# Performance work log

Measured on AMD Instinct MI355X. Metric: run time of the kernel, lower is better.

Reference implementation:

```python
import jax, jax.numpy as jnp
import numpy as np

B, D, H = 262144, 250, 100  # batch, input_length, hidden_length


def setup_inputs() -> dict:
    key = jax.random.key(0)
    ks = jax.random.split(key, 20)
    s_in = 1.0 / np.sqrt(D)
    s_h = 1.0 / np.sqrt(H)
    inp = {
        "x": jax.random.normal(ks[0], (B, D), jnp.float32),
        "h_prev": jax.random.normal(ks[1], (B, H), jnp.float32),
        "h_shared_prev": jax.random.normal(ks[2], (B, H), jnp.float32),
        # shared nn.GRUCell(D, H) params (torch layout: weight_ih [3H, D], weight_hh [3H, H])
        "Wi": jax.random.uniform(ks[3], (3 * H, D), jnp.float32, -s_in, s_in),
        "Wh": jax.random.uniform(ks[4], (3 * H, H), jnp.float32, -s_h, s_h),
        "bi": jax.random.uniform(ks[5], (3 * H,), jnp.float32, -s_h, s_h),
        "bh": jax.random.uniform(ks[6], (3 * H,), jnp.float32, -s_h, s_h),
        # task-specific bias-free linears, torch nn.Linear layout [out, in]
        "W_z": jax.random.uniform(ks[7], (H, D), jnp.float32, -s_in, s_in),
        "U_z": jax.random.uniform(ks[8], (H, H), jnp.float32, -s_h, s_h),
        "Us_z": jax.random.uniform(ks[9], (H, H), jnp.float32, -s_h, s_h),
        "W_r": jax.random.uniform(ks[10], (H, D), jnp.float32, -s_in, s_in),
        "U_r": jax.random.uniform(ks[11], (H, H), jnp.float32, -s_h, s_h),
        "Us_r": jax.random.uniform(ks[12], (H, H), jnp.float32, -s_h, s_h),
        "W_hn": jax.random.uniform(ks[13], (H, D), jnp.float32, -s_in, s_in),
        "U_hn": jax.random.uniform(ks[14], (H, H), jnp.float32, -s_h, s_h),
        "Us_hn": jax.random.uniform(ks[15], (H, H), jnp.float32, -s_h, s_h),
    }
    return inp


def _shared_gru_cell(x, h, Wi, Wh, bi, bh):
    # standard torch nn.GRUCell math
    gi = x @ Wi.T + bi          # [B, 3H]
    gh = h @ Wh.T + bh          # [B, 3H]
    i_r, i_z, i_n = jnp.split(gi, 3, axis=-1)
    h_r, h_z, h_n = jnp.split(gh, 3, axis=-1)
    r = jax.nn.sigmoid(i_r + h_r)
    z = jax.nn.sigmoid(i_z + h_z)
    n = jnp.tanh(i_n + r * h_n)
    return (1.0 - z) * n + z * h


def reference(x, h_prev, h_shared_prev, Wi, Wh, bi, bh,
              W_z, U_z, Us_z, W_r, U_r, Us_r, W_hn, U_hn, Us_hn):
    h_shared_new = _shared_gru_cell(x, h_shared_prev, Wi, Wh, bi, bh)
    z = jax.nn.sigmoid(x @ W_z.T + h_prev @ U_z.T + h_shared_new @ Us_z.T)
    r = jax.nn.sigmoid(x @ W_r.T + h_prev @ U_r.T + h_shared_new @ Us_r.T)
    nm = jnp.tanh(x @ W_hn.T + r * (h_prev @ U_hn.T) + h_shared_new @ Us_hn.T)
    h_new = (1.0 - z) * nm + z * h_prev
    return h_new
```

## Files before the change

kernel.cpp:

```cpp
#include <hip/hip_runtime.h>
#include <stdint.h>

#define D_IN 250
#define H_DIM 100
#define RPW 32
#define NTHREADS 256
#define BM (4*RPW)

#define P2_FRAG 252
#define TOTAL_E ((252 + 336) * 512)

typedef __bf16 bf16x8 __attribute__((ext_vector_type(8)));
typedef float f32x4 __attribute__((ext_vector_type(4)));

static __device__ __forceinline__ uint16_t f2bf(float f) {
  uint32_t u = __builtin_bit_cast(uint32_t, f);
  u = (u + 0x7FFFu + ((u >> 16) & 1u)) >> 16;
  return (uint16_t)u;
}
static __device__ __forceinline__ float bf2f(uint16_t h) {
  uint32_t u = ((uint32_t)h) << 16;
  return __builtin_bit_cast(float, u);
}
static __device__ __forceinline__ float sigmoidf_(float x) {
  return 1.0f / (1.0f + __expf(-x));
}
static __device__ __forceinline__ float tanhf_(float x) {
  return 2.0f / (1.0f + __expf(-2.0f * x)) - 1.0f;
}

__global__ void prepack_kernel(const float* __restrict__ Wi, const float* __restrict__ Wh,
                               const float* __restrict__ W_z, const float* __restrict__ U_z,
                               const float* __restrict__ Us_z, const float* __restrict__ W_r,
                               const float* __restrict__ U_r, const float* __restrict__ Us_r,
                               const float* __restrict__ W_hn, const float* __restrict__ U_hn,
                               const float* __restrict__ Us_hn, const float* __restrict__ bi,
                               const float* __restrict__ bh, uint16_t* __restrict__ ws) {
  int idx = blockIdx.x * blockDim.x + threadIdx.x;
  if (idx >= TOTAL_E) return;
  int f = idx >> 9;
  int a = idx & 511;
  int lane = a >> 3, j = a & 7;
  int kloc = ((lane >> 4) << 3) + j;
  int cl = lane & 15;
  float val = 0.f;
  if (f < P2_FRAG) {
    int g = f % 3, ks = (f / 3) % 12, t = f / 36;
    int c = t * 16 + cl;
    if (c < H_DIM) {
      if (ks < 8) {
        int k = ks * 32 + kloc;
        if (k < D_IN)       val = Wi[(size_t)(g * H_DIM + c) * D_IN + k];
        else if (k == D_IN) val = bi[g * H_DIM + c];
      } else {
        int k = (ks - 8) * 32 + kloc;
        if (k < H_DIM)       val = Wh[(size_t)(g * H_DIM + c) * H_DIM + k];
        else if (k == H_DIM) val = bh[g * H_DIM + c];
      }
    }
  } else {
    int f2 = f - P2_FRAG;
    int g = f2 % 3, ks = (f2 / 3) % 16, t = f2 / 48;
    int c = t * 16 + cl;
    if (c < H_DIM) {
      if (ks < 8) {
        int k = ks * 32 + kloc;
        const float* W = g == 0 ? W_z : g == 1 ? W_r : W_hn;
        if (k < D_IN) val = W[(size_t)c * D_IN + k];
      } else if (ks < 12) {
        int k = (ks - 8) * 32 + kloc;
        const float* W = g == 0 ? U_z : g == 1 ? U_r : U_hn;
        if (k < H_DIM) val = W[(size_t)c * H_DIM + k];
      } else {
        int k = (ks - 12) * 32 + kloc;
        const float* W = g == 0 ? Us_z : g == 1 ? Us_r : Us_hn;
        if (k < H_DIM) val = W[(size_t)c * H_DIM + k];
      }
    }
  }
  ws[idx] = f2bf(val);
}

static __device__ __forceinline__ bf16x8 xfrag(const float* __restrict__ xr, int ks, int q) {
  int c0 = ks * 32 + q * 8;
  bf16x8 a;
  if (c0 < 248) {
    #pragma unroll
    for (int i = 0; i < 4; ++i) {
      float2 f = *(const float2*)(xr + c0 + 2 * i);
      a[2 * i] = (__bf16)f.x; a[2 * i + 1] = (__bf16)f.y;
    }
  } else {
    float2 f = *(const float2*)(xr + 248);
    a[0] = (__bf16)f.x; a[1] = (__bf16)f.y; a[2] = (__bf16)1.0f;
    a[3] = (__bf16)0.0f; a[4] = (__bf16)0.0f; a[5] = (__bf16)0.0f;
    a[6] = (__bf16)0.0f; a[7] = (__bf16)0.0f;
  }
  return a;
}
static __device__ __forceinline__ bf16x8 hfrag(const float* __restrict__ hr, int ks, int q, float bias) {
  int c0 = ks * 32 + q * 8;
  bf16x8 a;
  #pragma unroll
  for (int i = 0; i < 8; ++i) a[i] = (__bf16)0.0f;
  if (c0 <= 88) {
    #pragma unroll
    for (int i = 0; i < 4; ++i) {
      float2 f = *(const float2*)(hr + c0 + 2 * i);
      a[2 * i] = (__bf16)f.x; a[2 * i + 1] = (__bf16)f.y;
    }
  } else if (c0 == 96) {
    float2 f0 = *(const float2*)(hr + 96);
    float2 f1 = *(const float2*)(hr + 98);
    a[0] = (__bf16)f0.x; a[1] = (__bf16)f0.y; a[2] = (__bf16)f1.x; a[3] = (__bf16)f1.y;
    a[4] = (__bf16)bias;
  }
  return a;
}

#define MFMA(A, B, C) __builtin_amdgcn_mfma_f32_16x16x32_bf16((A), (B), (C), 0, 0, 0)

typedef const __attribute__((address_space(1))) unsigned int* gp1_t;
typedef __attribute__((address_space(3))) unsigned int* lp3_t;

static __device__ __forceinline__ void gload(const uint16_t* gsrc, uint16_t* ldst) {
  __builtin_amdgcn_global_load_lds((gp1_t)gsrc, (lp3_t)ldst, 16, 0, 0);
}
#define WAIT_VM5   asm volatile("s_waitcnt vmcnt(5)" ::: "memory")
#define WAIT_LGKM0 asm volatile("s_waitcnt lgkmcnt(0)" ::: "memory")
#define BAR        do { __builtin_amdgcn_s_barrier(); __builtin_amdgcn_sched_barrier(0); } while (0)

__global__ __launch_bounds__(NTHREADS, 2) void gru_fused(
    const float* __restrict__ x, const float* __restrict__ hp_g,
    const float* __restrict__ hs_g, const uint16_t* __restrict__ ws,
    float* __restrict__ out) {
  __shared__ __align__(16) uint16_t ldsT[4 * RPW * 128];
  __shared__ __align__(16) uint16_t ring[8 * 1536];

  const int tid = threadIdx.x;
  const int lane = tid & 63, wid = tid >> 6;
  const int q = lane >> 4, cl = lane & 15;
  const int rowbase = blockIdx.x * BM + wid * RPW;
  uint16_t* lT = ldsT + wid * (RPW * 128);
  const uint16_t* wsl = ws + lane * 8;

  bf16x8 xa[2][8], ha[2][4], pa[2][4];
  #pragma unroll
  for (int h = 0; h < 2; ++h) {
    const float* xr = x + (size_t)(rowbase + h * 16 + cl) * D_IN;
    #pragma unroll
    for (int ks = 0; ks < 8; ++ks) xa[h][ks] = xfrag(xr, ks, q);
    const float* hr = hs_g + (size_t)(rowbase + h * 16 + cl) * H_DIM;
    #pragma unroll
    for (int ks = 0; ks < 4; ++ks) ha[h][ks] = hfrag(hr, ks, q, 1.0f);
    const float* pr = hp_g + (size_t)(rowbase + h * 16 + cl) * H_DIM;
    #pragma unroll
    for (int ks = 0; ks < 4; ++ks) pa[h][ks] = hfrag(pr, ks, q, 0.0f);
  }

  #pragma unroll
  for (int h = 0; h < 2; ++h) {
    int row = h * 16 + cl;
    #pragma unroll
    for (int ks = 0; ks < 4; ++ks) {
      int bo = row * 256 + (((ks * 64) + q * 16) ^ ((row & 7) << 4));
      *(bf16x8*)((char*)lT + bo) = ha[h][ks];
    }
  }

  if (wid < 3) {
    #pragma unroll
    for (int s = 0; s < 6; ++s)
      gload(wsl + (size_t)(s * 3 + wid) * 512, ring + s * 1536 + wid * 512);
    WAIT_VM5;
  }
  BAR;

  #pragma unroll 1
  for (int t = 0; t < 7; ++t) {
    f32x4 aR[2], aZ[2], aNi[2], aNh[2];
    #pragma unroll
    for (int h = 0; h < 2; ++h) { aR[h] = (f32x4)(0.f); aZ[h] = (f32x4)(0.f); aNi[h] = (f32x4)(0.f); aNh[h] = (f32x4)(0.f); }
    #pragma unroll
    for (int ks = 0; ks < 12; ++ks) {
      const uint16_t* sp = ring + ((t * 12 + ks) & 7) * 1536 + lane * 8;
      bf16x8 b0 = *(const bf16x8*)(sp);
      bf16x8 b1 = *(const bf16x8*)(sp + 512);
      bf16x8 b2 = *(const bf16x8*)(sp + 1024);
      if (wid < 3) {
        int fid = (ks < 6) ? (t * 36 + (ks + 6) * 3)
                : (t < 6 ? ((t + 1) * 36 + (ks - 6) * 3) : (P2_FRAG + (ks - 6) * 3));
        gload(wsl + (size_t)(fid + wid) * 512,
              ring + ((t * 12 + ks + 6) & 7) * 1536 + wid * 512);
      }
      #pragma unroll
      for (int h = 0; h < 2; ++h) {
        bf16x8 av = (ks < 8) ? xa[h][ks] : ha[h][ks - 8];
        aR[h] = MFMA(av, b0, aR[h]);
        aZ[h] = MFMA(av, b1, aZ[h]);
        if (ks < 8) aNi[h] = MFMA(av, b2, aNi[h]);
        else        aNh[h] = MFMA(av, b2, aNh[h]);
      }
      if (wid < 3) WAIT_VM5;
      BAR;
    }
    int c = t * 16 + cl;
    #pragma unroll
    for (int h = 0; h < 2; ++h) {
      #pragma unroll
      for (int r = 0; r < 4; ++r) {
        int row = h * 16 + q * 4 + r;
        int bo = row * 256 + ((c * 2) ^ ((row & 7) << 4));
        float hsp = bf2f(*(const uint16_t*)((const char*)lT + bo));
        float rr = sigmoidf_(aR[h][r]);
        float zz = sigmoidf_(aZ[h][r]);
        float nn = tanhf_(aNi[h][r] + rr * aNh[h][r]);
        float hsn = (1.f - zz) * nn + zz * hsp;
        *(uint16_t*)((char*)lT + bo) = f2bf(hsn);
      }
    }
  }

  bf16x8 na[2][4];
  #pragma unroll
  for (int h = 0; h < 2; ++h) {
    int row = h * 16 + cl;
    #pragma unroll
    for (int ks = 0; ks < 4; ++ks) {
      int bo = row * 256 + (((ks * 64) + q * 16) ^ ((row & 7) << 4));
      na[h][ks] = *(const bf16x8*)((const char*)lT + bo);
    }
  }
  WAIT_LGKM0;
  #pragma unroll
  for (int h = 0; h < 2; ++h) {
    int row = h * 16 + cl;
    #pragma unroll
    for (int ks = 0; ks < 4; ++ks) {
      int bo = row * 256 + (((ks * 64) + q * 16) ^ ((row & 7) << 4));
      *(bf16x8*)((char*)lT + bo) = pa[h][ks];
    }
  }

  #pragma unroll 1
  for (int t = 0; t < 7; ++t) {
    f32x4 aZ[2], aR[2], aNa[2], aNb[2];
    #pragma unroll
    for (int h = 0; h < 2; ++h) { aZ[h] = (f32x4)(0.f); aR[h] = (f32x4)(0.f); aNa[h] = (f32x4)(0.f); aNb[h] = (f32x4)(0.f); }
    #pragma unroll
    for (int ks = 0; ks < 16; ++ks) {
      const uint16_t* sp = ring + ((84 + t * 16 + ks) & 7) * 1536 + lane * 8;
      bf16x8 b0 = *(const bf16x8*)(sp);
      bf16x8 b1 = *(const bf16x8*)(sp + 512);
      bf16x8 b2 = *(const bf16x8*)(sp + 1024);
      if (wid < 3) {
        int fid = (ks < 10) ? (P2_FRAG + t * 48 + (ks + 6) * 3)
                : (t < 6 ? (P2_FRAG + (t + 1) * 48 + (ks - 10) * 3)
                         : (P2_FRAG + 6 * 48 + 15 * 3));
        gload(wsl + (size_t)(fid + wid) * 512,
              ring + ((84 + t * 16 + ks + 6) & 7) * 1536 + wid * 512);
      }
      #pragma unroll
      for (int h = 0; h < 2; ++h) {
        bf16x8 av = (ks < 8) ? xa[h][ks] : (ks < 12) ? pa[h][ks - 8] : na[h][ks - 12];
        aZ[h] = MFMA(av, b0, aZ[h]);
        aR[h] = MFMA(av, b1, aR[h]);
        if (ks < 8)       aNa[h] = MFMA(av, b2, aNa[h]);
        else if (ks < 12) aNb[h] = MFMA(av, b2, aNb[h]);
        else              aNa[h] = MFMA(av, b2, aNa[h]);
      }
      if (wid < 3) WAIT_VM5;
      BAR;
    }
    int c = t * 16 + cl;
    bool valid = c < H_DIM;
    #pragma unroll
    for (int h = 0; h < 2; ++h) {
      #pragma unroll
      for (int r = 0; r < 4; ++r) {
        int row = h * 16 + q * 4 + r;
        int bo = row * 256 + ((c * 2) ^ ((row & 7) << 4));
        float hpv = bf2f(*(const uint16_t*)((const char*)lT + bo));
        float z2 = sigmoidf_(aZ[h][r]);
        float r2 = sigmoidf_(aR[h][r]);
        float nm = tanhf_(aNa[h][r] + r2 * aNb[h][r]);
        float hnew = (1.f - z2) * nm + z2 * hpv;
        if (valid) out[(size_t)(rowbase + row) * H_DIM + c] = hnew;
      }
    }
  }
}

extern "C" void kernel_launch(void* const* d_in, const int* in_sizes, int n_in,
                              void* d_out, int out_size, void* d_ws, size_t ws_size,
                              hipStream_t stream) {
  const float* x    = (const float*)d_in[0];
  const float* h_p  = (const float*)d_in[1];
  const float* h_s  = (const float*)d_in[2];
  const float* Wi   = (const float*)d_in[3];
  const float* Wh   = (const float*)d_in[4];
  const float* bi   = (const float*)d_in[5];
  const float* bh   = (const float*)d_in[6];
  const float* W_z  = (const float*)d_in[7];
  const float* U_z  = (const float*)d_in[8];
  const float* Us_z = (const float*)d_in[9];
  const float* W_r  = (const float*)d_in[10];
  const float* U_r  = (const float*)d_in[11];
  const float* Us_r = (const float*)d_in[12];
  const float* W_hn = (const float*)d_in[13];
  const float* U_hn = (const float*)d_in[14];
  const float* Us_hn= (const float*)d_in[15];
  uint16_t* ws = (uint16_t*)d_ws;
  float* out = (float*)d_out;

  int rows = in_sizes[0] / D_IN;
  prepack_kernel<<<(TOTAL_E + 255) / 256, 256, 0, stream>>>(
      Wi, Wh, W_z, U_z, Us_z, W_r, U_r, Us_r, W_hn, U_hn, Us_hn, bi, bh, ws);
  gru_fused<<<rows / BM, NTHREADS, 0, stream>>>(x, h_p, h_s, ws, out);
}
```

Baseline: 272.0 us.

## Shrink weight ring to six slots, pair k-steps per barrier, raise occupancy

```diff
diff --git a/kernel.cpp b/kernel.cpp
--- a/kernel.cpp
+++ b/kernel.cpp
@@ -9,6 +9,8 @@
 
 #define P2_FRAG 252
 #define TOTAL_E ((252 + 336) * 512)
+
+#define NSLOT 6
 
 typedef __bf16 bf16x8 __attribute__((ext_vector_type(8)));
 typedef float f32x4 __attribute__((ext_vector_type(4)));
@@ -126,16 +128,21 @@
 static __device__ __forceinline__ void gload(const uint16_t* gsrc, uint16_t* ldst) {
   __builtin_amdgcn_global_load_lds((gp1_t)gsrc, (lp3_t)ldst, 16, 0, 0);
 }
-#define WAIT_VM5   asm volatile("s_waitcnt vmcnt(5)" ::: "memory")
+#define WAIT_VM2   asm volatile("s_waitcnt vmcnt(2)" ::: "memory")
 #define WAIT_LGKM0 asm volatile("s_waitcnt lgkmcnt(0)" ::: "memory")
 #define BAR        do { __builtin_amdgcn_s_barrier(); __builtin_amdgcn_sched_barrier(0); } while (0)
 
-__global__ __launch_bounds__(NTHREADS, 2) void gru_fused(
+static __device__ __forceinline__ int adv(int s, int n) {
+  s += n;
+  return s >= NSLOT ? s - NSLOT : s;
+}
+
+__global__ __launch_bounds__(NTHREADS, 3) void gru_fused(
     const float* __restrict__ x, const float* __restrict__ hp_g,
     const float* __restrict__ hs_g, const uint16_t* __restrict__ ws,
     float* __restrict__ out) {
   __shared__ __align__(16) uint16_t ldsT[4 * RPW * 128];
-  __shared__ __align__(16) uint16_t ring[8 * 1536];
+  __shared__ __align__(16) uint16_t ring[NSLOT * 1536];
 
   const int tid = threadIdx.x;
   const int lane = tid & 63, wid = tid >> 6;
@@ -170,11 +177,13 @@
 
   if (wid < 3) {
     #pragma unroll
-    for (int s = 0; s < 6; ++s)
+    for (int s = 0; s < 4; ++s)
       gload(wsl + (size_t)(s * 3 + wid) * 512, ring + s * 1536 + wid * 512);
-    WAIT_VM5;
+    WAIT_VM2;
   }
   BAR;
+
+  int cslot = 0, islot = 4;
 
   #pragma unroll 1
   for (int t = 0; t < 7; ++t) {
@@ -182,26 +191,48 @@
     #pragma unroll
     for (int h = 0; h < 2; ++h) { aR[h] = (f32x4)(0.f); aZ[h] = (f32x4)(0.f); aNi[h] = (f32x4)(0.f); aNh[h] = (f32x4)(0.f); }
     #pragma unroll
-    for (int ks = 0; ks < 12; ++ks) {
-      const uint16_t* sp = ring + ((t * 12 + ks) & 7) * 1536 + lane * 8;
-      bf16x8 b0 = *(const bf16x8*)(sp);
-      bf16x8 b1 = *(const bf16x8*)(sp + 512);
-      bf16x8 b2 = *(const bf16x8*)(sp + 1024);
+    for (int ks = 0; ks < 12; ks += 2) {
+      int c0s = cslot, c1s = adv(cslot, 1);
+      const uint16_t* spa = ring + c0s * 1536 + lane * 8;
+      bf16x8 a0 = *(const bf16x8*)(spa);
+      bf16x8 a1 = *(const bf16x8*)(spa + 512);
+      bf16x8 a2 = *(const bf16x8*)(spa + 1024);
       if (wid < 3) {
-        int fid = (ks < 6) ? (t * 36 + (ks + 6) * 3)
-                : (t < 6 ? ((t + 1) * 36 + (ks - 6) * 3) : (P2_FRAG + (ks - 6) * 3));
-        gload(wsl + (size_t)(fid + wid) * 512,
-              ring + ((t * 12 + ks + 6) & 7) * 1536 + wid * 512);
-      }
+        int f1 = (ks + 4 < 12) ? (t * 36 + (ks + 4) * 3)
+               : (t < 6 ? ((t + 1) * 36 + (ks - 8) * 3) : (P2_FRAG + (ks - 8) * 3));
+        gload(wsl + (size_t)(f1 + wid) * 512, ring + islot * 1536 + wid * 512);
+      }
+      __builtin_amdgcn_s_setprio(1);
       #pragma unroll
       for (int h = 0; h < 2; ++h) {
         bf16x8 av = (ks < 8) ? xa[h][ks] : ha[h][ks - 8];
+        aR[h] = MFMA(av, a0, aR[h]);
+        aZ[h] = MFMA(av, a1, aZ[h]);
+        if (ks < 8) aNi[h] = MFMA(av, a2, aNi[h]);
+        else        aNh[h] = MFMA(av, a2, aNh[h]);
+      }
+      __builtin_amdgcn_s_setprio(0);
+      const uint16_t* spb = ring + c1s * 1536 + lane * 8;
+      bf16x8 b0 = *(const bf16x8*)(spb);
+      bf16x8 b1 = *(const bf16x8*)(spb + 512);
+      bf16x8 b2 = *(const bf16x8*)(spb + 1024);
+      if (wid < 3) {
+        int f2_ = (ks + 5 < 12) ? (t * 36 + (ks + 5) * 3)
+                : (t < 6 ? ((t + 1) * 36 + (ks - 7) * 3) : (P2_FRAG + (ks - 7) * 3));
+        gload(wsl + (size_t)(f2_ + wid) * 512, ring + adv(islot, 1) * 1536 + wid * 512);
+      }
+      __builtin_amdgcn_s_setprio(1);
+      #pragma unroll
+      for (int h = 0; h < 2; ++h) {
+        bf16x8 av = (ks + 1 < 8) ? xa[h][ks + 1] : ha[h][ks + 1 - 8];
         aR[h] = MFMA(av, b0, aR[h]);
         aZ[h] = MFMA(av, b1, aZ[h]);
-        if (ks < 8) aNi[h] = MFMA(av, b2, aNi[h]);
-        else        aNh[h] = MFMA(av, b2, aNh[h]);
-      }
-      if (wid < 3) WAIT_VM5;
+        if (ks + 1 < 8) aNi[h] = MFMA(av, b2, aNi[h]);
+        else            aNh[h] = MFMA(av, b2, aNh[h]);
+      }
+      __builtin_amdgcn_s_setprio(0);
+      cslot = adv(cslot, 2); islot = adv(islot, 2);
+      if (wid < 3) WAIT_VM2;
       BAR;
     }
     int c = t * 16 + cl;
@@ -248,28 +279,50 @@
     #pragma unroll
     for (int h = 0; h < 2; ++h) { aZ[h] = (f32x4)(0.f); aR[h] = (f32x4)(0.f); aNa[h] = (f32x4)(0.f); aNb[h] = (f32x4)(0.f); }
     #pragma unroll
-    for (int ks = 0; ks < 16; ++ks) {
-      const uint16_t* sp = ring + ((84 + t * 16 + ks) & 7) * 1536 + lane * 8;
-      bf16x8 b0 = *(const bf16x8*)(sp);
-      bf16x8 b1 = *(const bf16x8*)(sp + 512);
-      bf16x8 b2 = *(const bf16x8*)(sp + 1024);
+    for (int ks = 0; ks < 16; ks += 2) {
+      int c0s = cslot, c1s = adv(cslot, 1);
+      const uint16_t* spa = ring + c0s * 1536 + lane * 8;
+      bf16x8 a0 = *(const bf16x8*)(spa);
+      bf16x8 a1 = *(const bf16x8*)(spa + 512);
+      bf16x8 a2 = *(const bf16x8*)(spa + 1024);
       if (wid < 3) {
-        int fid = (ks < 10) ? (P2_FRAG + t * 48 + (ks + 6) * 3)
-                : (t < 6 ? (P2_FRAG + (t + 1) * 48 + (ks - 10) * 3)
-                         : (P2_FRAG + 6 * 48 + 15 * 3));
-        gload(wsl + (size_t)(fid + wid) * 512,
-              ring + ((84 + t * 16 + ks + 6) & 7) * 1536 + wid * 512);
-      }
+        int f1 = (ks + 4 < 16) ? (P2_FRAG + t * 48 + (ks + 4) * 3)
+               : (t < 6 ? (P2_FRAG + (t + 1) * 48 + (ks - 12) * 3) : (P2_FRAG + 6 * 48 + 45));
+        gload(wsl + (size_t)(f1 + wid) * 512, ring + islot * 1536 + wid * 512);
+      }
+      __builtin_amdgcn_s_setprio(1);
       #pragma unroll
       for (int h = 0; h < 2; ++h) {
         bf16x8 av = (ks < 8) ? xa[h][ks] : (ks < 12) ? pa[h][ks - 8] : na[h][ks - 12];
+        aZ[h] = MFMA(av, a0, aZ[h]);
+        aR[h] = MFMA(av, a1, aR[h]);
+        if (ks < 8)       aNa[h] = MFMA(av, a2, aNa[h]);
+        else if (ks < 12) aNb[h] = MFMA(av, a2, aNb[h]);
+        else              aNa[h] = MFMA(av, a2, aNa[h]);
+      }
+      __builtin_amdgcn_s_setprio(0);
+      const uint16_t* spb = ring + c1s * 1536 + lane * 8;
+      bf16x8 b0 = *(const bf16x8*)(spb);
+      bf16x8 b1 = *(const bf16x8*)(spb + 512);
+      bf16x8 b2 = *(const bf16x8*)(spb + 1024);
+      if (wid < 3) {
+        int f2_ = (ks + 5 < 16) ? (P2_FRAG + t * 48 + (ks + 5) * 3)
+                : (t < 6 ? (P2_FRAG + (t + 1) * 48 + (ks - 11) * 3) : (P2_FRAG + 6 * 48 + 45));
+        gload(wsl + (size_t)(f2_ + wid) * 512, ring + adv(islot, 1) * 1536 + wid * 512);
+      }
+      __builtin_amdgcn_s_setprio(1);
+      #pragma unroll
+      for (int h = 0; h < 2; ++h) {
+        bf16x8 av = (ks + 1 < 8) ? xa[h][ks + 1] : (ks + 1 < 12) ? pa[h][ks + 1 - 8] : na[h][ks + 1 - 12];
         aZ[h] = MFMA(av, b0, aZ[h]);
         aR[h] = MFMA(av, b1, aR[h]);
-        if (ks < 8)       aNa[h] = MFMA(av, b2, aNa[h]);
-        else if (ks < 12) aNb[h] = MFMA(av, b2, aNb[h]);
-        else              aNa[h] = MFMA(av, b2, aNa[h]);
-      }
-      if (wid < 3) WAIT_VM5;
+        if (ks + 1 < 8)       aNa[h] = MFMA(av, b2, aNa[h]);
+        else if (ks + 1 < 12) aNb[h] = MFMA(av, b2, aNb[h]);
+        else                  aNa[h] = MFMA(av, b2, aNa[h]);
+      }
+      __builtin_amdgcn_s_setprio(0);
+      cslot = adv(cslot, 2); islot = adv(islot, 2);
+      if (wid < 3) WAIT_VM2;
       BAR;
     }
     int c = t * 16 + cl;
```

New measurement: 497.5 us. 82.9% more time.

## Restructure weight ring to 12 slots with grouped 4-step stages and fewer barriers

Applied to the files above, without the earlier changes.

```diff
diff --git a/kernel.cpp b/kernel.cpp
--- a/kernel.cpp
+++ b/kernel.cpp
@@ -9,6 +9,8 @@
 
 #define P2_FRAG 252
 #define TOTAL_E ((252 + 336) * 512)
+
+#define NSLOT 12
 
 typedef __bf16 bf16x8 __attribute__((ext_vector_type(8)));
 typedef float f32x4 __attribute__((ext_vector_type(4)));
@@ -126,7 +128,7 @@
 static __device__ __forceinline__ void gload(const uint16_t* gsrc, uint16_t* ldst) {
   __builtin_amdgcn_global_load_lds((gp1_t)gsrc, (lp3_t)ldst, 16, 0, 0);
 }
-#define WAIT_VM5   asm volatile("s_waitcnt vmcnt(5)" ::: "memory")
+#define WAIT_VM3   asm volatile("s_waitcnt vmcnt(3)" ::: "memory")
 #define WAIT_LGKM0 asm volatile("s_waitcnt lgkmcnt(0)" ::: "memory")
 #define BAR        do { __builtin_amdgcn_s_barrier(); __builtin_amdgcn_sched_barrier(0); } while (0)
 
@@ -135,7 +137,7 @@
     const float* __restrict__ hs_g, const uint16_t* __restrict__ ws,
     float* __restrict__ out) {
   __shared__ __align__(16) uint16_t ldsT[4 * RPW * 128];
-  __shared__ __align__(16) uint16_t ring[8 * 1536];
+  __shared__ __align__(16) uint16_t ring[NSLOT * 1536];
 
   const int tid = threadIdx.x;
   const int lane = tid & 63, wid = tid >> 6;
@@ -168,11 +170,16 @@
     }
   }
 
-  if (wid < 3) {
-    #pragma unroll
-    for (int s = 0; s < 6; ++s)
-      gload(wsl + (size_t)(s * 3 + wid) * 512, ring + s * 1536 + wid * 512);
-    WAIT_VM5;
+  {
+    int f0 = wid * 3;
+    #pragma unroll
+    for (int gg = 0; gg < 3; ++gg)
+      gload(wsl + (size_t)(f0 + gg) * 512, ring + wid * 1536 + gg * 512);
+    int f1 = (4 + wid) * 3;
+    #pragma unroll
+    for (int gg = 0; gg < 3; ++gg)
+      gload(wsl + (size_t)(f1 + gg) * 512, ring + (4 + wid) * 1536 + gg * 512);
+    WAIT_VM3;
   }
   BAR;
 
@@ -182,26 +189,34 @@
     #pragma unroll
     for (int h = 0; h < 2; ++h) { aR[h] = (f32x4)(0.f); aZ[h] = (f32x4)(0.f); aNi[h] = (f32x4)(0.f); aNh[h] = (f32x4)(0.f); }
     #pragma unroll
-    for (int ks = 0; ks < 12; ++ks) {
-      const uint16_t* sp = ring + ((t * 12 + ks) & 7) * 1536 + lane * 8;
-      bf16x8 b0 = *(const bf16x8*)(sp);
-      bf16x8 b1 = *(const bf16x8*)(sp + 512);
-      bf16x8 b2 = *(const bf16x8*)(sp + 1024);
-      if (wid < 3) {
-        int fid = (ks < 6) ? (t * 36 + (ks + 6) * 3)
-                : (t < 6 ? ((t + 1) * 36 + (ks - 6) * 3) : (P2_FRAG + (ks - 6) * 3));
-        gload(wsl + (size_t)(fid + wid) * 512,
-              ring + ((t * 12 + ks + 6) & 7) * 1536 + wid * 512);
-      }
-      #pragma unroll
-      for (int h = 0; h < 2; ++h) {
-        bf16x8 av = (ks < 8) ? xa[h][ks] : ha[h][ks - 8];
-        aR[h] = MFMA(av, b0, aR[h]);
-        aZ[h] = MFMA(av, b1, aZ[h]);
-        if (ks < 8) aNi[h] = MFMA(av, b2, aNi[h]);
-        else        aNh[h] = MFMA(av, b2, aNh[h]);
-      }
-      if (wid < 3) WAIT_VM5;
+    for (int g = 0; g < 3; ++g) {
+      int islot = (g == 0) ? (8 + wid) : (g == 1) ? wid : (4 + wid);
+      int fid;
+      if (g == 0)      fid = t * 36 + (8 + wid) * 3;
+      else if (g == 1) fid = (t < 6) ? ((t + 1) * 36 + wid * 3) : (P2_FRAG + wid * 3);
+      else             fid = (t < 6) ? ((t + 1) * 36 + (4 + wid) * 3) : (P2_FRAG + (4 + wid) * 3);
+      #pragma unroll
+      for (int gg = 0; gg < 3; ++gg)
+        gload(wsl + (size_t)(fid + gg) * 512, ring + islot * 1536 + gg * 512);
+      #pragma unroll
+      for (int so = 0; so < 4; ++so) {
+        const int ks = 4 * g + so;
+        const uint16_t* sp = ring + ks * 1536 + lane * 8;
+        bf16x8 b0 = *(const bf16x8*)(sp);
+        bf16x8 b1 = *(const bf16x8*)(sp + 512);
+        bf16x8 b2 = *(const bf16x8*)(sp + 1024);
+        __builtin_amdgcn_s_setprio(1);
+        #pragma unroll
+        for (int h = 0; h < 2; ++h) {
+          bf16x8 av = (ks < 8) ? xa[h][ks] : ha[h][ks - 8];
+          aR[h] = MFMA(av, b0, aR[h]);
+          aZ[h] = MFMA(av, b1, aZ[h]);
+          if (ks < 8) aNi[h] = MFMA(av, b2, aNi[h]);
+          else        aNh[h] = MFMA(av, b2, aNh[h]);
+        }
+        __builtin_amdgcn_s_setprio(0);
+      }
+      WAIT_VM3;
       BAR;
     }
     int c = t * 16 + cl;
@@ -242,34 +257,49 @@
     }
   }
 
+  int sb = 0;
   #pragma unroll 1
   for (int t = 0; t < 7; ++t) {
     f32x4 aZ[2], aR[2], aNa[2], aNb[2];
     #pragma unroll
     for (int h = 0; h < 2; ++h) { aZ[h] = (f32x4)(0.f); aR[h] = (f32x4)(0.f); aNa[h] = (f32x4)(0.f); aNb[h] = (f32x4)(0.f); }
     #pragma unroll
-    for (int ks = 0; ks < 16; ++ks) {
-      const uint16_t* sp = ring + ((84 + t * 16 + ks) & 7) * 1536 + lane * 8;
-      bf16x8 b0 = *(const bf16x8*)(sp);
-      bf16x8 b1 = *(const bf16x8*)(sp + 512);
-      bf16x8 b2 = *(const bf16x8*)(sp + 1024);
-      if (wid < 3) {
-        int fid = (ks < 10) ? (P2_FRAG + t * 48 + (ks + 6) * 3)
-                : (t < 6 ? (P2_FRAG + (t + 1) * 48 + (ks - 10) * 3)
-                         : (P2_FRAG + 6 * 48 + 15 * 3));
-        gload(wsl + (size_t)(fid + wid) * 512,
-              ring + ((84 + t * 16 + ks + 6) & 7) * 1536 + wid * 512);
-      }
-      #pragma unroll
-      for (int h = 0; h < 2; ++h) {
-        bf16x8 av = (ks < 8) ? xa[h][ks] : (ks < 12) ? pa[h][ks - 8] : na[h][ks - 12];
-        aZ[h] = MFMA(av, b0, aZ[h]);
-        aR[h] = MFMA(av, b1, aR[h]);
-        if (ks < 8)       aNa[h] = MFMA(av, b2, aNa[h]);
-        else if (ks < 12) aNb[h] = MFMA(av, b2, aNb[h]);
-        else              aNa[h] = MFMA(av, b2, aNa[h]);
-      }
-      if (wid < 3) WAIT_VM5;
+    for (int g = 0; g < 4; ++g) {
+      int fid;
+      if (g == 0)      fid = P2_FRAG + t * 48 + (8 + wid) * 3;
+      else if (g == 1) fid = P2_FRAG + t * 48 + (12 + wid) * 3;
+      else if (g == 2) fid = (t < 6) ? (P2_FRAG + (t + 1) * 48 + wid * 3) : P2_FRAG;
+      else             fid = (t < 6) ? (P2_FRAG + (t + 1) * 48 + (4 + wid) * 3) : P2_FRAG;
+      int islot = sb + 4 * g + 8 + wid;
+      if (islot >= NSLOT) islot -= NSLOT;
+      if (islot >= NSLOT) islot -= NSLOT;
+      #pragma unroll
+      for (int gg = 0; gg < 3; ++gg)
+        gload(wsl + (size_t)(fid + gg) * 512, ring + islot * 1536 + gg * 512);
+      int cb = sb + 4 * g;
+      if (cb >= NSLOT) cb -= NSLOT;
+      #pragma unroll
+      for (int so = 0; so < 4; ++so) {
+        const int ks = 4 * g + so;
+        int sl = cb + so;
+        if (sl >= NSLOT) sl -= NSLOT;
+        const uint16_t* sp = ring + sl * 1536 + lane * 8;
+        bf16x8 b0 = *(const bf16x8*)(sp);
+        bf16x8 b1 = *(const bf16x8*)(sp + 512);
+        bf16x8 b2 = *(const bf16x8*)(sp + 1024);
+        __builtin_amdgcn_s_setprio(1);
+        #pragma unroll
+        for (int h = 0; h < 2; ++h) {
+          bf16x8 av = (ks < 8) ? xa[h][ks] : (ks < 12) ? pa[h][ks - 8] : na[h][ks - 12];
+          aZ[h] = MFMA(av, b0, aZ[h]);
+          aR[h] = MFMA(av, b1, aR[h]);
+          if (ks < 8)       aNa[h] = MFMA(av, b2, aNa[h]);
+          else if (ks < 12) aNb[h] = MFMA(av, b2, aNb[h]);
+          else              aNa[h] = MFMA(av, b2, aNa[h]);
+        }
+        __builtin_amdgcn_s_setprio(0);
+      }
+      WAIT_VM3;
       BAR;
     }
     int c = t * 16 + cl;
@@ -288,6 +318,8 @@
         if (valid) out[(size_t)(rowbase + row) * H_DIM + c] = hnew;
       }
     }
+    sb += 4;
+    if (sb >= NSLOT) sb -= NSLOT;
   }
 }
 
```

After: 306.1 us. 1.13x slower.

## Double-buffer weight fragments in registers and halve barriers per K-step

Applied to the files above, without the earlier changes.

```diff
diff --git a/kernel.cpp b/kernel.cpp
--- a/kernel.cpp
+++ b/kernel.cpp
@@ -9,6 +9,8 @@
 
 #define P2_FRAG 252
 #define TOTAL_E ((252 + 336) * 512)
+
+#define NSLOT 8
 
 typedef __bf16 bf16x8 __attribute__((ext_vector_type(8)));
 typedef float f32x4 __attribute__((ext_vector_type(4)));
@@ -126,7 +128,8 @@
 static __device__ __forceinline__ void gload(const uint16_t* gsrc, uint16_t* ldst) {
   __builtin_amdgcn_global_load_lds((gp1_t)gsrc, (lp3_t)ldst, 16, 0, 0);
 }
-#define WAIT_VM5   asm volatile("s_waitcnt vmcnt(5)" ::: "memory")
+#define WAIT_VM2   asm volatile("s_waitcnt vmcnt(2)" ::: "memory")
+#define WAIT_VM0   asm volatile("s_waitcnt vmcnt(0)" ::: "memory")
 #define WAIT_LGKM0 asm volatile("s_waitcnt lgkmcnt(0)" ::: "memory")
 #define BAR        do { __builtin_amdgcn_s_barrier(); __builtin_amdgcn_sched_barrier(0); } while (0)
 
@@ -135,7 +138,7 @@
     const float* __restrict__ hs_g, const uint16_t* __restrict__ ws,
     float* __restrict__ out) {
   __shared__ __align__(16) uint16_t ldsT[4 * RPW * 128];
-  __shared__ __align__(16) uint16_t ring[8 * 1536];
+  __shared__ __align__(16) uint16_t ring[NSLOT * 1536];
 
   const int tid = threadIdx.x;
   const int lane = tid & 63, wid = tid >> 6;
@@ -172,36 +175,57 @@
     #pragma unroll
     for (int s = 0; s < 6; ++s)
       gload(wsl + (size_t)(s * 3 + wid) * 512, ring + s * 1536 + wid * 512);
-    WAIT_VM5;
+    WAIT_VM2;
   }
   BAR;
+
+  bf16x8 c00, c01, c02, c10, c11, c12;
+  {
+    const uint16_t* sp0 = ring + 0 * 1536 + lane * 8;
+    const uint16_t* sp1 = ring + 1 * 1536 + lane * 8;
+    c00 = *(const bf16x8*)(sp0); c01 = *(const bf16x8*)(sp0 + 512); c02 = *(const bf16x8*)(sp0 + 1024);
+    c10 = *(const bf16x8*)(sp1); c11 = *(const bf16x8*)(sp1 + 512); c12 = *(const bf16x8*)(sp1 + 1024);
+  }
 
   #pragma unroll 1
   for (int t = 0; t < 7; ++t) {
+    const int tb = (t & 1) << 2;
     f32x4 aR[2], aZ[2], aNi[2], aNh[2];
     #pragma unroll
     for (int h = 0; h < 2; ++h) { aR[h] = (f32x4)(0.f); aZ[h] = (f32x4)(0.f); aNi[h] = (f32x4)(0.f); aNh[h] = (f32x4)(0.f); }
     #pragma unroll
-    for (int ks = 0; ks < 12; ++ks) {
-      const uint16_t* sp = ring + ((t * 12 + ks) & 7) * 1536 + lane * 8;
-      bf16x8 b0 = *(const bf16x8*)(sp);
-      bf16x8 b1 = *(const bf16x8*)(sp + 512);
-      bf16x8 b2 = *(const bf16x8*)(sp + 1024);
+    for (int ks = 0; ks < 12; ks += 2) {
       if (wid < 3) {
-        int fid = (ks < 6) ? (t * 36 + (ks + 6) * 3)
-                : (t < 6 ? ((t + 1) * 36 + (ks - 6) * 3) : (P2_FRAG + (ks - 6) * 3));
-        gload(wsl + (size_t)(fid + wid) * 512,
-              ring + ((t * 12 + ks + 6) & 7) * 1536 + wid * 512);
-      }
+        const int k6 = ks + 6, k7 = ks + 7;
+        int f6 = (k6 < 12) ? (t * 36 + k6 * 3)
+               : (t < 6 ? ((t + 1) * 36 + (k6 - 12) * 3) : (P2_FRAG + (k6 - 12) * 3));
+        int f7 = (k7 < 12) ? (t * 36 + k7 * 3)
+               : (t < 6 ? ((t + 1) * 36 + (k7 - 12) * 3) : (P2_FRAG + (k7 - 12) * 3));
+        gload(wsl + (size_t)(f6 + wid) * 512, ring + ((tb + ks + 6) & 7) * 1536 + wid * 512);
+        gload(wsl + (size_t)(f7 + wid) * 512, ring + ((tb + ks + 7) & 7) * 1536 + wid * 512);
+      }
+      __builtin_amdgcn_s_setprio(1);
       #pragma unroll
       for (int h = 0; h < 2; ++h) {
-        bf16x8 av = (ks < 8) ? xa[h][ks] : ha[h][ks - 8];
-        aR[h] = MFMA(av, b0, aR[h]);
-        aZ[h] = MFMA(av, b1, aZ[h]);
-        if (ks < 8) aNi[h] = MFMA(av, b2, aNi[h]);
-        else        aNh[h] = MFMA(av, b2, aNh[h]);
-      }
-      if (wid < 3) WAIT_VM5;
+        bf16x8 av0 = (ks < 8) ? xa[h][ks] : ha[h][ks - 8];
+        aR[h] = MFMA(av0, c00, aR[h]);
+        aZ[h] = MFMA(av0, c01, aZ[h]);
+        if (ks < 8) aNi[h] = MFMA(av0, c02, aNi[h]);
+        else        aNh[h] = MFMA(av0, c02, aNh[h]);
+        bf16x8 av1 = (ks + 1 < 8) ? xa[h][ks + 1] : ha[h][ks + 1 - 8];
+        aR[h] = MFMA(av1, c10, aR[h]);
+        aZ[h] = MFMA(av1, c11, aZ[h]);
+        if (ks + 1 < 8) aNi[h] = MFMA(av1, c12, aNi[h]);
+        else            aNh[h] = MFMA(av1, c12, aNh[h]);
+      }
+      __builtin_amdgcn_s_setprio(0);
+      {
+        const uint16_t* sp0 = ring + ((tb + ks + 2) & 7) * 1536 + lane * 8;
+        const uint16_t* sp1 = ring + ((tb + ks + 3) & 7) * 1536 + lane * 8;
+        c00 = *(const bf16x8*)(sp0); c01 = *(const bf16x8*)(sp0 + 512); c02 = *(const bf16x8*)(sp0 + 1024);
+        c10 = *(const bf16x8*)(sp1); c11 = *(const bf16x8*)(sp1 + 512); c12 = *(const bf16x8*)(sp1 + 1024);
+      }
+      if (wid < 3) WAIT_VM2;
       BAR;
     }
     int c = t * 16 + cl;
@@ -248,28 +272,40 @@
     #pragma unroll
     for (int h = 0; h < 2; ++h) { aZ[h] = (f32x4)(0.f); aR[h] = (f32x4)(0.f); aNa[h] = (f32x4)(0.f); aNb[h] = (f32x4)(0.f); }
     #pragma unroll
-    for (int ks = 0; ks < 16; ++ks) {
-      const uint16_t* sp = ring + ((84 + t * 16 + ks) & 7) * 1536 + lane * 8;
-      bf16x8 b0 = *(const bf16x8*)(sp);
-      bf16x8 b1 = *(const bf16x8*)(sp + 512);
-      bf16x8 b2 = *(const bf16x8*)(sp + 1024);
+    for (int ks = 0; ks < 16; ks += 2) {
       if (wid < 3) {
-        int fid = (ks < 10) ? (P2_FRAG + t * 48 + (ks + 6) * 3)
-                : (t < 6 ? (P2_FRAG + (t + 1) * 48 + (ks - 10) * 3)
-                         : (P2_FRAG + 6 * 48 + 15 * 3));
-        gload(wsl + (size_t)(fid + wid) * 512,
-              ring + ((84 + t * 16 + ks + 6) & 7) * 1536 + wid * 512);
-      }
+        const int k6 = ks + 6, k7 = ks + 7;
+        int f6 = (k6 < 16) ? (P2_FRAG + t * 48 + k6 * 3)
+               : (t < 6 ? (P2_FRAG + (t + 1) * 48 + (k6 - 16) * 3) : P2_FRAG);
+        int f7 = (k7 < 16) ? (P2_FRAG + t * 48 + k7 * 3)
+               : (t < 6 ? (P2_FRAG + (t + 1) * 48 + (k7 - 16) * 3) : P2_FRAG);
+        gload(wsl + (size_t)(f6 + wid) * 512, ring + ((4 + ks + 6) & 7) * 1536 + wid * 512);
+        gload(wsl + (size_t)(f7 + wid) * 512, ring + ((4 + ks + 7) & 7) * 1536 + wid * 512);
+      }
+      __builtin_amdgcn_s_setprio(1);
       #pragma unroll
       for (int h = 0; h < 2; ++h) {
-        bf16x8 av = (ks < 8) ? xa[h][ks] : (ks < 12) ? pa[h][ks - 8] : na[h][ks - 12];
-        aZ[h] = MFMA(av, b0, aZ[h]);
-        aR[h] = MFMA(av, b1, aR[h]);
-        if (ks < 8)       aNa[h] = MFMA(av, b2, aNa[h]);
-        else if (ks < 12) aNb[h] = MFMA(av, b2, aNb[h]);
-        else              aNa[h] = MFMA(av, b2, aNa[h]);
-      }
-      if (wid < 3) WAIT_VM5;
+        bf16x8 av0 = (ks < 8) ? xa[h][ks] : (ks < 12) ? pa[h][ks - 8] : na[h][ks - 12];
+        aZ[h] = MFMA(av0, c00, aZ[h]);
+        aR[h] = MFMA(av0, c01, aR[h]);
+        if (ks < 8)       aNa[h] = MFMA(av0, c02, aNa[h]);
+        else if (ks < 12) aNb[h] = MFMA(av0, c02, aNb[h]);
+        else              aNa[h] = MFMA(av0, c02, aNa[h]);
+        bf16x8 av1 = (ks + 1 < 8) ? xa[h][ks + 1] : (ks + 1 < 12) ? pa[h][ks + 1 - 8] : na[h][ks + 1 - 12];
+        aZ[h] = MFMA(av1, c10, aZ[h]);
+        aR[h] = MFMA(av1, c11, aR[h]);
+        if (ks + 1 < 8)       aNa[h] = MFMA(av1, c12, aNa[h]);
+        else if (ks + 1 < 12) aNb[h] = MFMA(av1, c12, aNb[h]);
+        else                  aNa[h] = MFMA(av1, c12, aNa[h]);
+      }
+      __builtin_amdgcn_s_setprio(0);
+      {
+        const uint16_t* sp0 = ring + ((4 + ks + 2) & 7) * 1536 + lane * 8;
+        const uint16_t* sp1 = ring + ((4 + ks + 3) & 7) * 1536 + lane * 8;
+        c00 = *(const bf16x8*)(sp0); c01 = *(const bf16x8*)(sp0 + 512); c02 = *(const bf16x8*)(sp0 + 1024);
+        c10 = *(const bf16x8*)(sp1); c11 = *(const bf16x8*)(sp1 + 512); c12 = *(const bf16x8*)(sp1 + 1024);
+      }
+      if (wid < 3) WAIT_VM2;
       BAR;
     }
     int c = t * 16 + cl;
@@ -289,6 +325,8 @@
       }
     }
   }
+
+  WAIT_VM0;
 }
 
 extern "C" void kernel_launch(void* const* d_in, const int* in_sizes, int n_in,
```

Measured after the change: 271.1 us. No clear change (-0.3%).
